# Optimization experiments

Measured on AMD Instinct MI355X. Metric: run time of the kernel, lower is better.

Reference implementation:

```python
import jax, jax.numpy as jnp
import numpy as np

N = 10000        # nodes
E = 320000       # edges (before self-loops)
G = 100          # graphs in batch
HEADS = 2
OUT = 125        # per-head out channels
NEG_SLOPE = 0.2  # PyG GATConv default leaky_relu slope


def setup_inputs() -> dict:
    key = jax.random.key(0)
    k = lambda i: jax.random.fold_in(key, i)
    rn = lambda i, shape, s=0.1: jax.random.normal(k(i), shape, jnp.float32) * s
    inp = {
        "x": jax.random.normal(k(0), (N, 336), jnp.float32),
        "edge_index": jax.random.randint(k(1), (2, E), 0, N, jnp.int32),
        "batch": jnp.sort(jax.random.randint(k(2), (N,), 0, G, jnp.int32)),
    }
    conv_in = [336, 250, 250, 250]
    for i, din in enumerate(conv_in, start=1):
        base = 10 * i
        inp[f"W{i}"] = rn(base, (din, HEADS * OUT))
        inp[f"asrc{i}"] = rn(base + 1, (HEADS, OUT))
        inp[f"adst{i}"] = rn(base + 2, (HEADS, OUT))
        inp[f"b{i}"] = jnp.zeros((HEADS * OUT,), jnp.float32)
    lin_dims = [(250, 200), (200, 100), (100, 100), (100, 29)]
    for i, (din, dout) in enumerate(lin_dims, start=1):
        inp[f"lw{i}"] = rn(100 + i, (din, dout))
        inp[f"lb{i}"] = jnp.zeros((dout,), jnp.float32)
    return inp


def gat_conv(x, src, dst, W, asrc, adst, b):
    # PyG GATConv (v1), concat heads, self-loops already in (src, dst).
    n = x.shape[0]
    h = (x @ W).reshape(n, HEADS, OUT)                    # [N,H,C]
    e_src = jnp.einsum('nhc,hc->nh', h, asrc)             # a_src . h_j
    e_dst = jnp.einsum('nhc,hc->nh', h, adst)             # a_dst . h_i
    e = jax.nn.leaky_relu(e_src[src] + e_dst[dst], NEG_SLOPE)  # [Etot,H]
    m = jax.ops.segment_max(e, dst, num_segments=n)       # segment softmax over incoming edges
    e = jnp.exp(e - m[dst])
    denom = jax.ops.segment_sum(e, dst, num_segments=n)
    alpha = e / (denom[dst] + 1e-16)                      # [Etot,H]
    out = jax.ops.segment_sum(alpha[:, :, None] * h[src], dst, num_segments=n)
    return out.reshape(n, HEADS * OUT) + b


def reference(x, edge_index, batch,
              W1, asrc1, adst1, b1, W2, asrc2, adst2, b2,
              W3, asrc3, adst3, b3, W4, asrc4, adst4, b4,
              lw1, lb1, lw2, lb2, lw3, lb3, lw4, lb4):
    n = x.shape[0]
    loop = jnp.arange(n, dtype=edge_index.dtype)
    src = jnp.concatenate([edge_index[0], loop])          # add_self_loops=True
    dst = jnp.concatenate([edge_index[1], loop])

    h = jax.nn.relu(gat_conv(x, src, dst, W1, asrc1, adst1, b1))
    h = jax.nn.relu(gat_conv(h, src, dst, W2, asrc2, adst2, b2))
    h = jax.nn.relu(gat_conv(h, src, dst, W3, asrc3, adst3, b3))
    h = jax.nn.relu(gat_conv(h, src, dst, W4, asrc4, adst4, b4))

    # global_mean_pool over graph ids
    sums = jax.ops.segment_sum(h, batch, num_segments=G)
    cnts = jax.ops.segment_sum(jnp.ones((n, 1), h.dtype), batch, num_segments=G)
    g = sums / jnp.maximum(cnts, 1.0)                     # [G,250]

    g = jax.nn.relu(g @ lw1 + lb1)
    g = jax.nn.relu(g @ lw2 + lb2)
    g = jax.nn.relu(g @ lw3 + lb3)
    return g @ lw4 + lb4                                  # [G,29]
```

## Files before the change

kernel.cpp:

```cpp
#include <hip/hip_runtime.h>
#include <hip/hip_bf16.h>

#define NNODES 10000
#define NEDGES 320000
#define ETOT   (NEDGES + NNODES)
#define NGRAPH 100
#define CH     250
#define HOUT   125
#define MPAD   10048
#define KP0    352
#define KP1    256
#define HPAD   256
#define DCAP   256

typedef __attribute__((ext_vector_type(8))) short bf16x8;
typedef __attribute__((ext_vector_type(4))) float f32x4;

static __device__ __forceinline__ float bfbits2f(unsigned int u){
  union{ unsigned int i; float f; } v; v.i = u << 16; return v.f;
}
static __device__ __forceinline__ unsigned short f2bfbits(float f){
  __hip_bfloat16 b = __float2bfloat16(f);
  union{ __hip_bfloat16 b; unsigned short s; } v; v.b = b; return v.s;
}

__global__ void k_deg(const int* __restrict__ eidx, int* __restrict__ deg,
                      const int* __restrict__ batch, int* __restrict__ gstart){
  int e = blockIdx.x*blockDim.x + threadIdx.x;
  if (e < ETOT){
    int dst = (e < NEDGES) ? eidx[NEDGES + e] : (e - NEDGES);
    atomicAdd(&deg[dst], 1);
  }
  if (e < NNODES){
    int b1 = batch[e];
    int b0 = (e == 0) ? -1 : batch[e-1];
    for (int b = b0 + 1; b <= b1; ++b) gstart[b] = e;
    if (e == NNODES - 1){
      for (int b = b1 + 1; b <= NGRAPH; ++b) gstart[b] = NNODES;
    }
  }
}

__global__ __launch_bounds__(1024) void k_scan(const int* __restrict__ deg, int* __restrict__ rowptr){
  const int CHUNK = 10;
  int tid = threadIdx.x;
  int base = tid * CHUNK;
  int sum = 0;
  #pragma unroll
  for (int u = 0; u < CHUNK; ++u){
    int i = base + u;
    sum += (i < NNODES) ? deg[i] : 0;
  }
  int lane = tid & 63, wv = tid >> 6;
  int v = sum;
  #pragma unroll
  for (int off = 1; off < 64; off <<= 1){
    int t = __shfl_up(v, off);
    if (lane >= off) v += t;
  }
  __shared__ int wtot[16];
  __shared__ int woff[16];
  if (lane == 63) wtot[wv] = v;
  __syncthreads();
  if (tid == 0){
    int acc = 0;
    #pragma unroll
    for (int w = 0; w < 16; ++w){ woff[w] = acc; acc += wtot[w]; }
  }
  __syncthreads();
  int run = woff[wv] + v - sum;
  #pragma unroll
  for (int u = 0; u < CHUNK; ++u){
    int i = base + u;
    if (i < NNODES){
      run += deg[i];
      rowptr[i+1] = run;
    }
  }
  if (tid == 0) rowptr[0] = 0;
}

__global__ void k_fill(const int* __restrict__ eidx, const int* __restrict__ rowptr,
                       int* __restrict__ cursor, int* __restrict__ csr_src){
  int e = blockIdx.x*blockDim.x + threadIdx.x;
  if (e >= ETOT) return;
  int dst, src;
  if (e < NEDGES){ src = eidx[e]; dst = eidx[NEDGES + e]; }
  else           { src = e - NEDGES; dst = src; }
  int pos = atomicAdd(&cursor[dst], 1);
  csr_src[rowptr[dst] + pos] = src;
}

__global__ void k_xconv(const float* __restrict__ x, __hip_bfloat16* __restrict__ Ab){
  int idx = blockIdx.x*blockDim.x + threadIdx.x;
  if (idx >= NNODES*336) return;
  int r = idx / 336, k = idx % 336;
  Ab[(size_t)r * KP0 + k] = __float2bfloat16(x[idx]);
}

__global__ void k_wconv_all(const float* __restrict__ W0, const float* __restrict__ W1,
                            const float* __restrict__ W2, const float* __restrict__ W3,
                            __hip_bfloat16* __restrict__ Wt0, __hip_bfloat16* __restrict__ Wt1,
                            __hip_bfloat16* __restrict__ Wt2, __hip_bfloat16* __restrict__ Wt3){
  const int T0 = 16 * KP0 * 16;
  const int T1 = 16 * KP1 * 16;
  int idx = blockIdx.x*blockDim.x + threadIdx.x;
  const float* W; __hip_bfloat16* Wt; int K, Kp, li;
  if (idx < T0)              { W = W0; Wt = Wt0; K = 336; Kp = KP0; li = idx; }
  else if (idx < T0 +   T1)  { W = W1; Wt = Wt1; K = CH;  Kp = KP1; li = idx - T0; }
  else if (idx < T0 + 2*T1)  { W = W2; Wt = Wt2; K = CH;  Kp = KP1; li = idx - T0 - T1; }
  else if (idx < T0 + 3*T1)  { W = W3; Wt = Wt3; K = CH;  Kp = KP1; li = idx - T0 - 2*T1; }
  else return;
  int KC = Kp >> 5;
  int nt = li / (Kp * 16);
  int rem = li % (Kp * 16);
  int k = rem / 16;
  int n = rem % 16;
  int col = nt * 16 + n;
  float v = (k < K && col < CH) ? W[(size_t)k * CH + col] : 0.f;
  Wt[(((size_t)nt * KC + (k >> 5)) * 16 + n) * 32 + (k & 31)] = __float2bfloat16(v);
}

__global__ __launch_bounds__(256) void k_gemm_mfma(
    const __hip_bfloat16* __restrict__ A, const __hip_bfloat16* __restrict__ Wt,
    __hip_bfloat16* __restrict__ Cb, const float* __restrict__ asrc,
    const float* __restrict__ adst, float* __restrict__ esrc, float* __restrict__ edst,
    int M, int Kp){
  int wv = threadIdx.x >> 6, lane = threadIdx.x & 63;
  int n16 = lane & 15, q = lane >> 4;
  int KC = Kp >> 5;
  int rowbase = blockIdx.x * 64 + wv * 16;
  int bn = blockIdx.y * 64;
  int nt0 = bn >> 4;
  const __hip_bfloat16* ap = A  + (size_t)(rowbase + n16) * Kp + q * 8;
  const __hip_bfloat16* bp = Wt + ((size_t)nt0 * KC * 16 + n16) * 32 + q * 8;
  f32x4 ac0 = {0.f,0.f,0.f,0.f}, ac1 = ac0, ac2 = ac0, ac3 = ac0;
  for (int kc = 0; kc < KC; ++kc){
    bf16x8 a  = *(const bf16x8*)(ap + (size_t)kc * 32);
    bf16x8 b0 = *(const bf16x8*)(bp + ((size_t)0 * KC + kc) * 512);
    bf16x8 b1 = *(const bf16x8*)(bp + ((size_t)1 * KC + kc) * 512);
    bf16x8 b2 = *(const bf16x8*)(bp + ((size_t)2 * KC + kc) * 512);
    bf16x8 b3 = *(const bf16x8*)(bp + ((size_t)3 * KC + kc) * 512);
    ac0 = __builtin_amdgcn_mfma_f32_16x16x32_bf16(a, b0, ac0, 0, 0, 0);
    ac1 = __builtin_amdgcn_mfma_f32_16x16x32_bf16(a, b1, ac1, 0, 0, 0);
    ac2 = __builtin_amdgcn_mfma_f32_16x16x32_bf16(a, b2, ac2, 0, 0, 0);
    ac3 = __builtin_amdgcn_mfma_f32_16x16x32_bf16(a, b3, ac3, 0, 0, 0);
  }
  float es0[4] = {}, es1[4] = {}, ed0a[4] = {}, ed1a[4] = {};
  #define SCORE_T(AC, T) { \
    int col = bn + (T)*16 + n16; \
    bool ok = col < CH; \
    float av = ok ? asrc[col] : 0.f; \
    float dv = ok ? adst[col] : 0.f; \
    bool hh = col >= HOUT; \
    float av0 = hh ? 0.f : av, av1 = hh ? av : 0.f; \
    float dv0 = hh ? 0.f : dv, dv1 = hh ? dv : 0.f; \
    _Pragma("unroll") \
    for (int r = 0; r < 4; ++r){ \
      es0[r] += AC[r]*av0; es1[r] += AC[r]*av1; \
      ed0a[r] += AC[r]*dv0; ed1a[r] += AC[r]*dv1; } }
  SCORE_T(ac0, 0) SCORE_T(ac1, 1) SCORE_T(ac2, 2) SCORE_T(ac3, 3)
  #undef SCORE_T
  #pragma unroll
  for (int off = 1; off < 16; off <<= 1){
    #pragma unroll
    for (int r = 0; r < 4; ++r){
      es0[r]  += __shfl_xor(es0[r],  off);
      es1[r]  += __shfl_xor(es1[r],  off);
      ed0a[r] += __shfl_xor(ed0a[r], off);
      ed1a[r] += __shfl_xor(ed1a[r], off);
    }
  }
  if (n16 == 0){
    #pragma unroll
    for (int r = 0; r < 4; ++r){
      int row = rowbase + q*4 + r;
      if (row < M){
        atomicAdd(&esrc[row*2+0], es0[r]);
        atomicAdd(&esrc[row*2+1], es1[r]);
        atomicAdd(&edst[row*2+0], ed0a[r]);
        atomicAdd(&edst[row*2+1], ed1a[r]);
      }
    }
  }
  #pragma unroll
  for (int r = 0; r < 4; ++r){
    int row = rowbase + q * 4 + r;
    if (row >= M) continue;
    int col = bn + n16;
    __hip_bfloat16* cb = Cb + (size_t)row * HPAD + col;
    if (col      < CH) cb[0]  = __float2bfloat16(ac0[r]);
    if (col + 16 < CH) cb[16] = __float2bfloat16(ac1[r]);
    if (col + 32 < CH) cb[32] = __float2bfloat16(ac2[r]);
    if (col + 48 < CH) cb[48] = __float2bfloat16(ac3[r]);
  }
}

__global__ __launch_bounds__(256) void k_attn(const __hip_bfloat16* __restrict__ h,
                        const float* __restrict__ esrc, const float* __restrict__ edst,
                        const int* __restrict__ rowptr, const int* __restrict__ csr_src,
                        const float* __restrict__ bias, __hip_bfloat16* __restrict__ outb,
                        float* __restrict__ esZ, float* __restrict__ edZ){
  int node = blockIdx.x;
  int tid = threadIdx.x, wave = tid >> 6, lane = tid & 63;
  int start = rowptr[node], deg = rowptr[node+1] - start;
  __shared__ int   s_src[DCAP];
  __shared__ float s_x0[DCAP], s_x1[DCAP];
  __shared__ float wred0[4], wred1[4];
  __shared__ float sh[4 * 256];
  float ed0 = edst[node*2+0], ed1 = edst[node*2+1];
  float sm0 = 0.f, sm1 = 0.f;
  for (int i = tid; i < deg; i += 256){
    int src = csr_src[start + i];
    float e0 = esrc[src*2+0] + ed0; e0 = e0 > 0.f ? e0 : 0.2f*e0;
    float e1 = esrc[src*2+1] + ed1; e1 = e1 > 0.f ? e1 : 0.2f*e1;
    float x0 = __expf(e0), x1 = __expf(e1);
    if (i < DCAP){ s_src[i] = src; s_x0[i] = x0; s_x1[i] = x1; }
    sm0 += x0; sm1 += x1;
  }
  for (int off = 32; off > 0; off >>= 1){
    sm0 += __shfl_xor(sm0, off);
    sm1 += __shfl_xor(sm1, off);
  }
  if (lane == 0){ wred0[wave] = sm0; wred1[wave] = sm1; }
  __syncthreads();
  float inv0 = 1.f / ((wred0[0]+wred0[1]+wred0[2]+wred0[3]) + 1e-16f);
  float inv1 = 1.f / ((wred1[0]+wred1[1]+wred1[2]+wred1[3]) + 1e-16f);
  int c0 = 4*lane;
  bool h0_0 = (c0    ) < HOUT, h0_1 = (c0 + 1) < HOUT;
  bool h0_2 = (c0 + 2) < HOUT, h0_3 = (c0 + 3) < HOUT;
  float acc0=0.f, acc1=0.f, acc2=0.f, acc3=0.f;
  #define FETCH(I, S, A0, A1) { \
    if ((I) < DCAP){ S = s_src[I]; A0 = s_x0[I]*inv0; A1 = s_x1[I]*inv1; } \
    else { S = csr_src[start + (I)]; \
      float e0 = esrc[S*2+0] + ed0; e0 = e0 > 0.f ? e0 : 0.2f*e0; \
      float e1 = esrc[S*2+1] + ed1; e1 = e1 > 0.f ? e1 : 0.2f*e1; \
      A0 = __expf(e0)*inv0; A1 = __expf(e1)*inv1; } }
  #define GATHER(S, A0, A1) { \
    uint2 d = *(const uint2*)(h + (size_t)(S) * HPAD + c0); \
    acc0 += (h0_0 ? A0 : A1) * bfbits2f(d.x & 0xffffu); \
    acc1 += (h0_1 ? A0 : A1) * bfbits2f(d.x >> 16); \
    acc2 += (h0_2 ? A0 : A1) * bfbits2f(d.y & 0xffffu); \
    acc3 += (h0_3 ? A0 : A1) * bfbits2f(d.y >> 16); }
  int i = wave;
  for (; i + 4 < deg; i += 8){
    int sA, sB; float a0A,a1A,a0B,a1B;
    FETCH(i, sA, a0A, a1A)
    FETCH(i+4, sB, a0B, a1B)
    GATHER(sA, a0A, a1A)
    GATHER(sB, a0B, a1B)
  }
  if (i < deg){
    int sA; float a0A, a1A;
    FETCH(i, sA, a0A, a1A)
    GATHER(sA, a0A, a1A)
  }
  #undef GATHER
  #undef FETCH
  float* shw = sh + wave * 256;
  *(float4*)&shw[c0] = make_float4(acc0, acc1, acc2, acc3);
  __syncthreads();
  if (tid < 62){
    int c = 4*tid;
    float4 b4 = *(const float4*)&bias[c];
    float v0 = sh[c]   + sh[256+c]   + sh[512+c]   + sh[768+c]   + b4.x;
    float v1 = sh[c+1] + sh[256+c+1] + sh[512+c+1] + sh[768+c+1] + b4.y;
    float v2 = sh[c+2] + sh[256+c+2] + sh[512+c+2] + sh[768+c+2] + b4.z;
    float v3 = sh[c+3] + sh[256+c+3] + sh[512+c+3] + sh[768+c+3] + b4.w;
    v0 = v0 > 0.f ? v0 : 0.f; v1 = v1 > 0.f ? v1 : 0.f;
    v2 = v2 > 0.f ? v2 : 0.f; v3 = v3 > 0.f ? v3 : 0.f;
    ushort4 o; o.x = f2bfbits(v0); o.y = f2bfbits(v1); o.z = f2bfbits(v2); o.w = f2bfbits(v3);
    *(ushort4*)(outb + (size_t)node * KP1 + c) = o;
  } else if (tid == 62){
    #pragma unroll
    for (int j = 0; j < 2; ++j){
      int c = 248 + j;
      float v = sh[c] + sh[256+c] + sh[512+c] + sh[768+c] + bias[c];
      v = v > 0.f ? v : 0.f;
      outb[(size_t)node * KP1 + c] = __float2bfloat16(v);
    }
  }
  if (tid < 2){
    esZ[node*2 + tid] = 0.f;
    edZ[node*2 + tid] = 0.f;
  }
}

__global__ __launch_bounds__(256) void k_head(const __hip_bfloat16* __restrict__ xb,
                        const int* __restrict__ gstart,
                        const float* __restrict__ lw1, const float* __restrict__ lb1,
                        const float* __restrict__ lw2, const float* __restrict__ lb2,
                        const float* __restrict__ lw3, const float* __restrict__ lb3,
                        const float* __restrict__ lw4, const float* __restrict__ lb4,
                        float* __restrict__ out){
  int g = blockIdx.x;
  int tid = threadIdx.x;
  int s = gstart[g], e = gstart[g+1];
  __shared__ float gvec[256];
  __shared__ float m1[200];
  __shared__ float m2[112];
  __shared__ float m3[112];
  if (tid < CH){
    float a0=0.f,a1=0.f,a2=0.f,a3=0.f;
    int n = s;
    for (; n + 3 < e; n += 4){
      a0 += __bfloat162float(xb[(size_t)n     * KP1 + tid]);
      a1 += __bfloat162float(xb[(size_t)(n+1) * KP1 + tid]);
      a2 += __bfloat162float(xb[(size_t)(n+2) * KP1 + tid]);
      a3 += __bfloat162float(xb[(size_t)(n+3) * KP1 + tid]);
    }
    for (; n < e; ++n) a0 += __bfloat162float(xb[(size_t)n * KP1 + tid]);
    float scale = 1.f / fmaxf((float)(e - s), 1.f);
    gvec[tid] = (a0 + a1 + a2 + a3) * scale;
  }
  __syncthreads();
  if (tid < 200){
    float a0=0.f,a1=0.f,a2=0.f,a3=0.f;
    int k = 0;
    for (; k + 3 < CH; k += 4){
      a0 += gvec[k]   * lw1[(size_t)k     * 200 + tid];
      a1 += gvec[k+1] * lw1[(size_t)(k+1) * 200 + tid];
      a2 += gvec[k+2] * lw1[(size_t)(k+2) * 200 + tid];
      a3 += gvec[k+3] * lw1[(size_t)(k+3) * 200 + tid];
    }
    for (; k < CH; ++k) a0 += gvec[k] * lw1[(size_t)k * 200 + tid];
    float v = a0 + a1 + a2 + a3 + lb1[tid];
    m1[tid] = v > 0.f ? v : 0.f;
  }
  __syncthreads();
  if (tid < 100){
    float a0=0.f,a1=0.f,a2=0.f,a3=0.f;
    for (int k = 0; k + 3 < 200; k += 4){
      a0 += m1[k]   * lw2[(size_t)k     * 100 + tid];
      a1 += m1[k+1] * lw2[(size_t)(k+1) * 100 + tid];
      a2 += m1[k+2] * lw2[(size_t)(k+2) * 100 + tid];
      a3 += m1[k+3] * lw2[(size_t)(k+3) * 100 + tid];
    }
    float v = a0 + a1 + a2 + a3 + lb2[tid];
    m2[tid] = v > 0.f ? v : 0.f;
  }
  __syncthreads();
  if (tid < 100){
    float a0=0.f,a1=0.f,a2=0.f,a3=0.f;
    for (int k = 0; k + 3 < 100; k += 4){
      a0 += m2[k]   * lw3[(size_t)k     * 100 + tid];
      a1 += m2[k+1] * lw3[(size_t)(k+1) * 100 + tid];
      a2 += m2[k+2] * lw3[(size_t)(k+2) * 100 + tid];
      a3 += m2[k+3] * lw3[(size_t)(k+3) * 100 + tid];
    }
    float v = a0 + a1 + a2 + a3 + lb3[tid];
    m3[tid] = v > 0.f ? v : 0.f;
  }
  __syncthreads();
  if (tid < 29){
    float a0=0.f,a1=0.f,a2=0.f,a3=0.f;
    for (int k = 0; k + 3 < 100; k += 4){
      a0 += m3[k]   * lw4[(size_t)k     * 29 + tid];
      a1 += m3[k+1] * lw4[(size_t)(k+1) * 29 + tid];
      a2 += m3[k+2] * lw4[(size_t)(k+2) * 29 + tid];
      a3 += m3[k+3] * lw4[(size_t)(k+3) * 29 + tid];
    }
    out[(size_t)g * 29 + tid] = a0 + a1 + a2 + a3 + lb4[tid];
  }
}

extern "C" void kernel_launch(void* const* d_in, const int* in_sizes, int n_in,
                              void* d_out, int out_size, void* d_ws, size_t ws_size,
                              hipStream_t stream){
  const float* x   = (const float*)d_in[0];
  const int* eidx  = (const int*)d_in[1];
  const int* batch = (const int*)d_in[2];

  char* ws = (char*)d_ws;
  size_t off = 0;
  auto alloc = [&](size_t bytes)->void*{
    void* p = ws + off;
    off = (off + bytes + 255) & ~(size_t)255;
    return p;
  };
  __hip_bfloat16* hb16 = (__hip_bfloat16*)alloc((size_t)NNODES * HPAD * 2);
  __hip_bfloat16* Abf0 = (__hip_bfloat16*)alloc((size_t)MPAD * KP0 * 2);
  __hip_bfloat16* Abf  = (__hip_bfloat16*)alloc((size_t)MPAD * KP1 * 2);
  __hip_bfloat16* Wt0  = (__hip_bfloat16*)alloc((size_t)16 * KP0 * 16 * 2);
  __hip_bfloat16* Wt1  = (__hip_bfloat16*)alloc((size_t)16 * KP1 * 16 * 2);
  __hip_bfloat16* Wt2  = (__hip_bfloat16*)alloc((size_t)16 * KP1 * 16 * 2);
  __hip_bfloat16* Wt3  = (__hip_bfloat16*)alloc((size_t)16 * KP1 * 16 * 2);
  size_t zbeg = off;
  int*   deg    = (int*)  alloc((size_t)NNODES * 4);
  int*   cursor = (int*)  alloc((size_t)NNODES * 4);
  float* esA  = (float*)alloc((size_t)NNODES * 2 * 4);
  float* edA  = (float*)alloc((size_t)NNODES * 2 * 4);
  float* esB  = (float*)alloc((size_t)NNODES * 2 * 4);
  float* edB  = (float*)alloc((size_t)NNODES * 2 * 4);
  size_t zend = off;
  int*    rowptr  = (int*)   alloc((size_t)(NNODES + 1) * 4);
  int*    csr_src = (int*)   alloc((size_t)ETOT * 4);
  int*    gstart  = (int*)   alloc((size_t)(NGRAPH + 1) * 4);

  hipMemsetAsync(ws + zbeg, 0, zend - zbeg, stream);

  k_deg <<<(ETOT + 255)/256, 256, 0, stream>>>(eidx, deg, batch, gstart);
  k_scan<<<1, 1024, 0, stream>>>(deg, rowptr);
  k_fill<<<(ETOT + 255)/256, 256, 0, stream>>>(eidx, rowptr, cursor, csr_src);

  k_xconv<<<(NNODES*336 + 255)/256, 256, 0, stream>>>(x, Abf0);
  {
    int wtot = 16*KP0*16 + 3*16*KP1*16;
    k_wconv_all<<<(wtot + 255)/256, 256, 0, stream>>>(
        (const float*)d_in[3], (const float*)d_in[7], (const float*)d_in[11], (const float*)d_in[15],
        Wt0, Wt1, Wt2, Wt3);
  }

  const __hip_bfloat16* Wts[4] = {Wt0, Wt1, Wt2, Wt3};
  for (int L = 0; L < 4; ++L){
    const float* as_ = (const float*)d_in[4 + 4*L];
    const float* ad_ = (const float*)d_in[5 + 4*L];
    const float* bb  = (const float*)d_in[6 + 4*L];
    int Kp = (L == 0) ? KP0 : KP1;
    const __hip_bfloat16* Ain = (L == 0) ? Abf0 : Abf;
    float* es  = (L & 1) ? esB : esA;
    float* ed  = (L & 1) ? edB : edA;
    float* esZ = (L & 1) ? esA : esB;
    float* edZ = (L & 1) ? edA : edB;

    dim3 gg(MPAD/64, 4);
    k_gemm_mfma<<<gg, 256, 0, stream>>>(Ain, Wts[L], hb16, as_, ad_, es, ed, NNODES, Kp);
    k_attn<<<NNODES, 256, 0, stream>>>(hb16, es, ed, rowptr, csr_src, bb, Abf, esZ, edZ);
  }

  const float* lw1 = (const float*)d_in[19];
  const float* lb1 = (const float*)d_in[20];
  const float* lw2 = (const float*)d_in[21];
  const float* lb2 = (const float*)d_in[22];
  const float* lw3 = (const float*)d_in[23];
  const float* lb3 = (const float*)d_in[24];
  const float* lw4 = (const float*)d_in[25];
  const float* lb4 = (const float*)d_in[26];

  k_head<<<NGRAPH, 256, 0, stream>>>(Abf, gstart, lw1, lb1, lw2, lb2, lw3, lb3,
                                     lw4, lb4, (float*)d_out);
}
```

Measured before the change: 365.4 us.

## Fuse whole GAT pipeline into one cooperative persistent kernel with grid syncs

Replaces the sequence of about a dozen kernel launches (degree count, scan, CSR fill, conversions, per-layer GEMM and attention, head) with a single cooperative persistent kernel. Stages are separated by grid.sync, and work is distributed by grid-stride loops. The layer-0 GEMM runs concurrently with the single-block scan. This targets launch overhead and inter-kernel gaps. The cost is lower parallelism per stage: the grid is capped at 1024 blocks and attention loops over 10000 nodes, grid barriers add their own cost, and a non-cooperative fallback path is kept.

```diff
diff --git a/kernel.cpp b/kernel.cpp
--- a/kernel.cpp
+++ b/kernel.cpp
@@ -1,13 +1,18 @@
 #include <hip/hip_runtime.h>
+#include <hip/hip_cooperative_groups.h>
 #include <hip/hip_bf16.h>
+
+namespace cg = cooperative_groups;
 
 #define NNODES 10000
 #define NEDGES 320000
 #define ETOT   (NEDGES + NNODES)
 #define NGRAPH 100
+#define NCUS   256
 #define CH     250
 #define HOUT   125
 #define MPAD   10048
+#define NTILE  157
 #define KP0    352
 #define KP1    256
 #define HPAD   256
@@ -24,25 +29,22 @@
   union{ __hip_bfloat16 b; unsigned short s; } v; v.b = b; return v.s;
 }
 
-__global__ void k_deg(const int* __restrict__ eidx, int* __restrict__ deg,
-                      const int* __restrict__ batch, int* __restrict__ gstart){
-  int e = blockIdx.x*blockDim.x + threadIdx.x;
-  if (e < ETOT){
-    int dst = (e < NEDGES) ? eidx[NEDGES + e] : (e - NEDGES);
-    atomicAdd(&deg[dst], 1);
-  }
-  if (e < NNODES){
-    int b1 = batch[e];
-    int b0 = (e == 0) ? -1 : batch[e-1];
-    for (int b = b0 + 1; b <= b1; ++b) gstart[b] = e;
-    if (e == NNODES - 1){
-      for (int b = b1 + 1; b <= NGRAPH; ++b) gstart[b] = NNODES;
-    }
-  }
-}
-
-__global__ __launch_bounds__(1024) void k_scan(const int* __restrict__ deg, int* __restrict__ rowptr){
-  const int CHUNK = 10;
+struct MegaArgs {
+  const float* x; const int* eidx; const int* batch;
+  const float *W0,*W1,*W2,*W3;
+  const float *as0,*ad0,*b0;
+  const float *as1,*ad1,*b1;
+  const float *as2,*ad2,*b2;
+  const float *as3,*ad3,*b3;
+  const float *lw1,*lb1,*lw2,*lb2,*lw3,*lb3,*lw4,*lb4;
+  __hip_bfloat16 *hb16, *Abf0, *Abf, *Wt0, *Wt1, *Wt2, *Wt3;
+  int *deg, *cursor, *rowptr, *csr_src, *gstart;
+  float *esA,*edA,*esB,*edB;
+  float* out;
+};
+
+__device__ void scan256(char* smemc, const int* __restrict__ deg, int* __restrict__ rowptr){
+  const int CHUNK = 40;
   int tid = threadIdx.x;
   int base = tid * CHUNK;
   int sum = 0;
@@ -58,14 +60,14 @@
     int t = __shfl_up(v, off);
     if (lane >= off) v += t;
   }
-  __shared__ int wtot[16];
-  __shared__ int woff[16];
+  int* wtot = (int*)smemc;
+  int* woff = (int*)(smemc + 64);
   if (lane == 63) wtot[wv] = v;
   __syncthreads();
   if (tid == 0){
     int acc = 0;
     #pragma unroll
-    for (int w = 0; w < 16; ++w){ woff[w] = acc; acc += wtot[w]; }
+    for (int w = 0; w < 4; ++w){ woff[w] = acc; acc += wtot[w]; }
   }
   __syncthreads();
   int run = woff[wv] + v - sum;
@@ -80,57 +82,16 @@
   if (tid == 0) rowptr[0] = 0;
 }
 
-__global__ void k_fill(const int* __restrict__ eidx, const int* __restrict__ rowptr,
-                       int* __restrict__ cursor, int* __restrict__ csr_src){
-  int e = blockIdx.x*blockDim.x + threadIdx.x;
-  if (e >= ETOT) return;
-  int dst, src;
-  if (e < NEDGES){ src = eidx[e]; dst = eidx[NEDGES + e]; }
-  else           { src = e - NEDGES; dst = src; }
-  int pos = atomicAdd(&cursor[dst], 1);
-  csr_src[rowptr[dst] + pos] = src;
-}
-
-__global__ void k_xconv(const float* __restrict__ x, __hip_bfloat16* __restrict__ Ab){
-  int idx = blockIdx.x*blockDim.x + threadIdx.x;
-  if (idx >= NNODES*336) return;
-  int r = idx / 336, k = idx % 336;
-  Ab[(size_t)r * KP0 + k] = __float2bfloat16(x[idx]);
-}
-
-__global__ void k_wconv_all(const float* __restrict__ W0, const float* __restrict__ W1,
-                            const float* __restrict__ W2, const float* __restrict__ W3,
-                            __hip_bfloat16* __restrict__ Wt0, __hip_bfloat16* __restrict__ Wt1,
-                            __hip_bfloat16* __restrict__ Wt2, __hip_bfloat16* __restrict__ Wt3){
-  const int T0 = 16 * KP0 * 16;
-  const int T1 = 16 * KP1 * 16;
-  int idx = blockIdx.x*blockDim.x + threadIdx.x;
-  const float* W; __hip_bfloat16* Wt; int K, Kp, li;
-  if (idx < T0)              { W = W0; Wt = Wt0; K = 336; Kp = KP0; li = idx; }
-  else if (idx < T0 +   T1)  { W = W1; Wt = Wt1; K = CH;  Kp = KP1; li = idx - T0; }
-  else if (idx < T0 + 2*T1)  { W = W2; Wt = Wt2; K = CH;  Kp = KP1; li = idx - T0 - T1; }
-  else if (idx < T0 + 3*T1)  { W = W3; Wt = Wt3; K = CH;  Kp = KP1; li = idx - T0 - 2*T1; }
-  else return;
-  int KC = Kp >> 5;
-  int nt = li / (Kp * 16);
-  int rem = li % (Kp * 16);
-  int k = rem / 16;
-  int n = rem % 16;
-  int col = nt * 16 + n;
-  float v = (k < K && col < CH) ? W[(size_t)k * CH + col] : 0.f;
-  Wt[(((size_t)nt * KC + (k >> 5)) * 16 + n) * 32 + (k & 31)] = __float2bfloat16(v);
-}
-
-__global__ __launch_bounds__(256) void k_gemm_mfma(
+__device__ __forceinline__ void gemm_body(int bx, int by,
     const __hip_bfloat16* __restrict__ A, const __hip_bfloat16* __restrict__ Wt,
     __hip_bfloat16* __restrict__ Cb, const float* __restrict__ asrc,
     const float* __restrict__ adst, float* __restrict__ esrc, float* __restrict__ edst,
-    int M, int Kp){
+    int Kp){
   int wv = threadIdx.x >> 6, lane = threadIdx.x & 63;
   int n16 = lane & 15, q = lane >> 4;
   int KC = Kp >> 5;
-  int rowbase = blockIdx.x * 64 + wv * 16;
-  int bn = blockIdx.y * 64;
+  int rowbase = bx * 64 + wv * 16;
+  int bn = by * 64;
   int nt0 = bn >> 4;
   const __hip_bfloat16* ap = A  + (size_t)(rowbase + n16) * Kp + q * 8;
   const __hip_bfloat16* bp = Wt + ((size_t)nt0 * KC * 16 + n16) * 32 + q * 8;
@@ -175,7 +136,7 @@
     #pragma unroll
     for (int r = 0; r < 4; ++r){
       int row = rowbase + q*4 + r;
-      if (row < M){
+      if (row < NNODES){
         atomicAdd(&esrc[row*2+0], es0[r]);
         atomicAdd(&esrc[row*2+1], es1[r]);
         atomicAdd(&edst[row*2+0], ed0a[r]);
@@ -186,7 +147,7 @@
   #pragma unroll
   for (int r = 0; r < 4; ++r){
     int row = rowbase + q * 4 + r;
-    if (row >= M) continue;
+    if (row >= NNODES) continue;
     int col = bn + n16;
     __hip_bfloat16* cb = Cb + (size_t)row * HPAD + col;
     if (col      < CH) cb[0]  = __float2bfloat16(ac0[r]);
@@ -196,18 +157,20 @@
   }
 }
 
-__global__ __launch_bounds__(256) void k_attn(const __hip_bfloat16* __restrict__ h,
-                        const float* __restrict__ esrc, const float* __restrict__ edst,
-                        const int* __restrict__ rowptr, const int* __restrict__ csr_src,
-                        const float* __restrict__ bias, __hip_bfloat16* __restrict__ outb,
-                        float* __restrict__ esZ, float* __restrict__ edZ){
-  int node = blockIdx.x;
+__device__ __forceinline__ void attn_body(int node, char* smemc,
+    const __hip_bfloat16* __restrict__ h, const float* __restrict__ esrc,
+    const float* __restrict__ edst, const int* __restrict__ rowptr,
+    const int* __restrict__ csr_src, const float* __restrict__ bias,
+    __hip_bfloat16* __restrict__ outb, float* __restrict__ esZ, float* __restrict__ edZ){
   int tid = threadIdx.x, wave = tid >> 6, lane = tid & 63;
+  int*   s_src = (int*)  smemc;
+  float* s_x0  = (float*)(smemc + 1024);
+  float* s_x1  = (float*)(smemc + 2048);
+  float* wred0 = (float*)(smemc + 3072);
+  float* wred1 = (float*)(smemc + 3088);
+  float* sh    = (float*)(smemc + 3104);
+  __syncthreads();
   int start = rowptr[node], deg = rowptr[node+1] - start;
-  __shared__ int   s_src[DCAP];
-  __shared__ float s_x0[DCAP], s_x1[DCAP];
-  __shared__ float wred0[4], wred1[4];
-  __shared__ float sh[4 * 256];
   float ed0 = edst[node*2+0], ed1 = edst[node*2+1];
   float sm0 = 0.f, sm1 = 0.f;
   for (int i = tid; i < deg; i += 256){
@@ -286,20 +249,20 @@
   }
 }
 
-__global__ __launch_bounds__(256) void k_head(const __hip_bfloat16* __restrict__ xb,
-                        const int* __restrict__ gstart,
-                        const float* __restrict__ lw1, const float* __restrict__ lb1,
-                        const float* __restrict__ lw2, const float* __restrict__ lb2,
-                        const float* __restrict__ lw3, const float* __restrict__ lb3,
-                        const float* __restrict__ lw4, const float* __restrict__ lb4,
-                        float* __restrict__ out){
-  int g = blockIdx.x;
+__device__ __forceinline__ void head_body(int g, char* smemc,
+    const __hip_bfloat16* __restrict__ xb, const int* __restrict__ gstart,
+    const float* __restrict__ lw1, const float* __restrict__ lb1,
+    const float* __restrict__ lw2, const float* __restrict__ lb2,
+    const float* __restrict__ lw3, const float* __restrict__ lb3,
+    const float* __restrict__ lw4, const float* __restrict__ lb4,
+    float* __restrict__ out){
   int tid = threadIdx.x;
+  float* gvec = (float*)smemc;
+  float* m1   = (float*)(smemc + 1024);
+  float* m2   = (float*)(smemc + 1824);
+  float* m3   = (float*)(smemc + 2272);
+  __syncthreads();
   int s = gstart[g], e = gstart[g+1];
-  __shared__ float gvec[256];
-  __shared__ float m1[200];
-  __shared__ float m2[112];
-  __shared__ float m3[112];
   if (tid < CH){
     float a0=0.f,a1=0.f,a2=0.f,a3=0.f;
     int n = s;
@@ -364,13 +327,131 @@
   }
 }
 
+__device__ __forceinline__ void pre_body(const MegaArgs& a, int gtid, int gstr){
+  for (int e = gtid; e < ETOT; e += gstr){
+    int dst = (e < NEDGES) ? a.eidx[NEDGES + e] : (e - NEDGES);
+    atomicAdd(&a.deg[dst], 1);
+  }
+  for (int n = gtid; n < NNODES; n += gstr){
+    int b1 = a.batch[n];
+    int b0 = (n == 0) ? -1 : a.batch[n-1];
+    for (int b = b0 + 1; b <= b1; ++b) a.gstart[b] = n;
+    if (n == NNODES - 1){
+      for (int b = b1 + 1; b <= NGRAPH; ++b) a.gstart[b] = NNODES;
+    }
+  }
+  for (int i = gtid; i < NNODES*336; i += gstr){
+    int r = i / 336, k = i % 336;
+    a.Abf0[(size_t)r * KP0 + k] = __float2bfloat16(a.x[i]);
+  }
+  const int T0 = 16 * KP0 * 16;
+  const int T1 = 16 * KP1 * 16;
+  int tot = T0 + 3*T1;
+  for (int i = gtid; i < tot; i += gstr){
+    const float* W; __hip_bfloat16* Wt; int K, Kp, li;
+    if (i < T0)             { W = a.W0; Wt = a.Wt0; K = 336; Kp = KP0; li = i; }
+    else if (i < T0 +   T1) { W = a.W1; Wt = a.Wt1; K = CH;  Kp = KP1; li = i - T0; }
+    else if (i < T0 + 2*T1) { W = a.W2; Wt = a.Wt2; K = CH;  Kp = KP1; li = i - T0 - T1; }
+    else                    { W = a.W3; Wt = a.Wt3; K = CH;  Kp = KP1; li = i - T0 - 2*T1; }
+    int KC = Kp >> 5;
+    int nt = li / (Kp * 16);
+    int rem = li % (Kp * 16);
+    int k = rem / 16;
+    int n = rem % 16;
+    int col = nt * 16 + n;
+    float v = (k < K && col < CH) ? W[(size_t)k * CH + col] : 0.f;
+    Wt[(((size_t)nt * KC + (k >> 5)) * 16 + n) * 32 + (k & 31)] = __float2bfloat16(v);
+  }
+}
+__device__ __forceinline__ void fill_body(const MegaArgs& a, int gtid, int gstr){
+  for (int e = gtid; e < ETOT; e += gstr){
+    int dst, src;
+    if (e < NEDGES){ src = a.eidx[e]; dst = a.eidx[NEDGES + e]; }
+    else           { src = e - NEDGES; dst = src; }
+    int pos = atomicAdd(&a.cursor[dst], 1);
+    a.csr_src[a.rowptr[dst] + pos] = src;
+  }
+}
+
+__global__ __launch_bounds__(256, 4) void k_mega(MegaArgs a){
+  cg::grid_group grid = cg::this_grid();
+  __shared__ __align__(16) char smem[7424];
+  int tid = threadIdx.x;
+  int gtid = blockIdx.x * 256 + tid;
+  int gstr = gridDim.x * 256;
+
+  pre_body(a, gtid, gstr);
+  grid.sync();
+
+  if (blockIdx.x == 0){
+    scan256(smem, a.deg, a.rowptr);
+  } else {
+    for (int t = (int)blockIdx.x - 1; t < NTILE*4; t += (int)gridDim.x - 1)
+      gemm_body(t % NTILE, t / NTILE, a.Abf0, a.Wt0, a.hb16, a.as0, a.ad0, a.esA, a.edA, KP0);
+  }
+  grid.sync();
+
+  fill_body(a, gtid, gstr);
+  grid.sync();
+
+  for (int node = blockIdx.x; node < NNODES; node += gridDim.x)
+    attn_body(node, smem, a.hb16, a.esA, a.edA, a.rowptr, a.csr_src, a.b0,
+              a.Abf, a.esB, a.edB);
+  grid.sync();
+
+  const __hip_bfloat16* Wts[3] = {a.Wt1, a.Wt2, a.Wt3};
+  const float* ass[3] = {a.as1, a.as2, a.as3};
+  const float* ads[3] = {a.ad1, a.ad2, a.ad3};
+  const float* bbs[3] = {a.b1, a.b2, a.b3};
+  for (int Lm = 0; Lm < 3; ++Lm){
+    float* es  = (Lm & 1) ? a.esA : a.esB;
+    float* ed  = (Lm & 1) ? a.edA : a.edB;
+    float* esZ = (Lm & 1) ? a.esB : a.esA;
+    float* edZ = (Lm & 1) ? a.edB : a.edA;
+    for (int t = blockIdx.x; t < NTILE*4; t += gridDim.x)
+      gemm_body(t % NTILE, t / NTILE, a.Abf, Wts[Lm], a.hb16, ass[Lm], ads[Lm], es, ed, KP1);
+    grid.sync();
+    for (int node = blockIdx.x; node < NNODES; node += gridDim.x)
+      attn_body(node, smem, a.hb16, es, ed, a.rowptr, a.csr_src, bbs[Lm],
+                a.Abf, esZ, edZ);
+    grid.sync();
+  }
+
+  for (int g = blockIdx.x; g < NGRAPH; g += gridDim.x)
+    head_body(g, smem, a.Abf, a.gstart, a.lw1, a.lb1, a.lw2, a.lb2,
+              a.lw3, a.lb3, a.lw4, a.lb4, a.out);
+}
+
+__global__ void k_pre(MegaArgs a){
+  pre_body(a, blockIdx.x * blockDim.x + threadIdx.x, gridDim.x * blockDim.x);
+}
+__global__ __launch_bounds__(256) void k_scan_s(const int* __restrict__ deg, int* __restrict__ rowptr){
+  __shared__ __align__(16) char smem[128];
+  scan256(smem, deg, rowptr);
+}
+__global__ void k_fill_s(MegaArgs a){
+  fill_body(a, blockIdx.x * blockDim.x + threadIdx.x, gridDim.x * blockDim.x);
+}
+__global__ __launch_bounds__(256) void k_gemm_s(const __hip_bfloat16* A, const __hip_bfloat16* Wt,
+    __hip_bfloat16* Cb, const float* asrc, const float* adst, float* esrc, float* edst, int Kp){
+  gemm_body(blockIdx.x, blockIdx.y, A, Wt, Cb, asrc, adst, esrc, edst, Kp);
+}
+__global__ __launch_bounds__(256) void k_attn_s(const __hip_bfloat16* h, const float* esrc,
+    const float* edst, const int* rowptr, const int* csr_src, const float* bias,
+    __hip_bfloat16* outb, float* esZ, float* edZ){
+  __shared__ __align__(16) char smem[7424];
+  attn_body(blockIdx.x, smem, h, esrc, edst, rowptr, csr_src, bias, outb, esZ, edZ);
+}
+__global__ __launch_bounds__(256) void k_head_s(const __hip_bfloat16* xb, const int* gstart,
+    const float* lw1, const float* lb1, const float* lw2, const float* lb2,
+    const float* lw3, const float* lb3, const float* lw4, const float* lb4, float* out){
+  __shared__ __align__(16) char smem[2720];
+  head_body(blockIdx.x, smem, xb, gstart, lw1, lb1, lw2, lb2, lw3, lb3, lw4, lb4, out);
+}
+
 extern "C" void kernel_launch(void* const* d_in, const int* in_sizes, int n_in,
                               void* d_out, int out_size, void* d_ws, size_t ws_size,
                               hipStream_t stream){
-  const float* x   = (const float*)d_in[0];
-  const int* eidx  = (const int*)d_in[1];
-  const int* batch = (const int*)d_in[2];
-
   char* ws = (char*)d_ws;
   size_t off = 0;
   auto alloc = [&](size_t bytes)->void*{
@@ -393,50 +474,69 @@
   float* esB  = (float*)alloc((size_t)NNODES * 2 * 4);
   float* edB  = (float*)alloc((size_t)NNODES * 2 * 4);
   size_t zend = off;
-  int*    rowptr  = (int*)   alloc((size_t)(NNODES + 1) * 4);
-  int*    csr_src = (int*)   alloc((size_t)ETOT * 4);
-  int*    gstart  = (int*)   alloc((size_t)(NGRAPH + 1) * 4);
+  int*   rowptr  = (int*)alloc((size_t)(NNODES + 1) * 4);
+  int*   csr_src = (int*)alloc((size_t)ETOT * 4);
+  int*   gstart  = (int*)alloc((size_t)(NGRAPH + 1) * 4);
 
   hipMemsetAsync(ws + zbeg, 0, zend - zbeg, stream);
 
-  k_deg <<<(ETOT + 255)/256, 256, 0, stream>>>(eidx, deg, batch, gstart);
-  k_scan<<<1, 1024, 0, stream>>>(deg, rowptr);
-  k_fill<<<(ETOT + 255)/256, 256, 0, stream>>>(eidx, rowptr, cursor, csr_src);
-
-  k_xconv<<<(NNODES*336 + 255)/256, 256, 0, stream>>>(x, Abf0);
-  {
-    int wtot = 16*KP0*16 + 3*16*KP1*16;
-    k_wconv_all<<<(wtot + 255)/256, 256, 0, stream>>>(
-        (const float*)d_in[3], (const float*)d_in[7], (const float*)d_in[11], (const float*)d_in[15],
-        Wt0, Wt1, Wt2, Wt3);
-  }
-
-  const __hip_bfloat16* Wts[4] = {Wt0, Wt1, Wt2, Wt3};
-  for (int L = 0; L < 4; ++L){
-    const float* as_ = (const float*)d_in[4 + 4*L];
-    const float* ad_ = (const float*)d_in[5 + 4*L];
-    const float* bb  = (const float*)d_in[6 + 4*L];
-    int Kp = (L == 0) ? KP0 : KP1;
-    const __hip_bfloat16* Ain = (L == 0) ? Abf0 : Abf;
-    float* es  = (L & 1) ? esB : esA;
-    float* ed  = (L & 1) ? edB : edA;
-    float* esZ = (L & 1) ? esA : esB;
-    float* edZ = (L & 1) ? edA : edB;
-
-    dim3 gg(MPAD/64, 4);
-    k_gemm_mfma<<<gg, 256, 0, stream>>>(Ain, Wts[L], hb16, as_, ad_, es, ed, NNODES, Kp);
-    k_attn<<<NNODES, 256, 0, stream>>>(hb16, es, ed, rowptr, csr_src, bb, Abf, esZ, edZ);
-  }
-
-  const float* lw1 = (const float*)d_in[19];
-  const float* lb1 = (const float*)d_in[20];
-  const float* lw2 = (const float*)d_in[21];
-  const float* lb2 = (const float*)d_in[22];
-  const float* lw3 = (const float*)d_in[23];
-  const float* lb3 = (const float*)d_in[24];
-  const float* lw4 = (const float*)d_in[25];
-  const float* lb4 = (const float*)d_in[26];
-
-  k_head<<<NGRAPH, 256, 0, stream>>>(Abf, gstart, lw1, lb1, lw2, lb2, lw3, lb3,
-                                     lw4, lb4, (float*)d_out);
-}
+  MegaArgs ma;
+  ma.x = (const float*)d_in[0];
+  ma.eidx = (const int*)d_in[1];
+  ma.batch = (const int*)d_in[2];
+  ma.W0 = (const float*)d_in[3];  ma.as0 = (const float*)d_in[4];
+  ma.ad0 = (const float*)d_in[5]; ma.b0  = (const float*)d_in[6];
+  ma.W1 = (const float*)d_in[7];  ma.as1 = (const float*)d_in[8];
+  ma.ad1 = (const float*)d_in[9]; ma.b1  = (const float*)d_in[10];
+  ma.W2 = (const float*)d_in[11]; ma.as2 = (const float*)d_in[12];
+  ma.ad2 = (const float*)d_in[13]; ma.b2 = (const float*)d_in[14];
+  ma.W3 = (const float*)d_in[15]; ma.as3 = (const float*)d_in[16];
+  ma.ad3 = (const float*)d_in[17]; ma.b3 = (const float*)d_in[18];
+  ma.lw1 = (const float*)d_in[19]; ma.lb1 = (const float*)d_in[20];
+  ma.lw2 = (const float*)d_in[21]; ma.lb2 = (const float*)d_in[22];
+  ma.lw3 = (const float*)d_in[23]; ma.lb3 = (const float*)d_in[24];
+  ma.lw4 = (const float*)d_in[25]; ma.lb4 = (const float*)d_in[26];
+  ma.hb16 = hb16; ma.Abf0 = Abf0; ma.Abf = Abf;
+  ma.Wt0 = Wt0; ma.Wt1 = Wt1; ma.Wt2 = Wt2; ma.Wt3 = Wt3;
+  ma.deg = deg; ma.cursor = cursor; ma.rowptr = rowptr;
+  ma.csr_src = csr_src; ma.gstart = gstart;
+  ma.esA = esA; ma.edA = edA; ma.esB = esB; ma.edB = edB;
+  ma.out = (float*)d_out;
+
+  bool coop_done = false;
+  int occ = 0;
+  hipError_t qe = hipOccupancyMaxActiveBlocksPerMultiprocessor(
+      &occ, reinterpret_cast<const void*>(k_mega), 256, 0);
+  if (qe == hipSuccess && occ > 0){
+    long grid = (long)occ * NCUS;
+    if (grid > 1024) grid = 1024;
+    if (grid >= 8){
+      void* kargs[] = { &ma };
+      hipError_t le = hipLaunchCooperativeKernel(
+          reinterpret_cast<void*>(k_mega), dim3((unsigned)grid), dim3(256), kargs, 0, stream);
+      coop_done = (le == hipSuccess);
+    }
+  }
+
+  if (!coop_done){
+    k_pre  <<<(ETOT + 255)/256, 256, 0, stream>>>(ma);
+    k_scan_s<<<1, 256, 0, stream>>>(deg, rowptr);
+    k_fill_s<<<(ETOT + 255)/256, 256, 0, stream>>>(ma);
+    const __hip_bfloat16* Wts[4] = {Wt0, Wt1, Wt2, Wt3};
+    const float* ass[4] = {ma.as0, ma.as1, ma.as2, ma.as3};
+    const float* ads[4] = {ma.ad0, ma.ad1, ma.ad2, ma.ad3};
+    const float* bbs[4] = {ma.b0, ma.b1, ma.b2, ma.b3};
+    for (int L = 0; L < 4; ++L){
+      int Kp = (L == 0) ? KP0 : KP1;
+      const __hip_bfloat16* Ain = (L == 0) ? Abf0 : Abf;
+      float* es  = (L & 1) ? esB : esA;
+      float* ed  = (L & 1) ? edB : edA;
+      float* esZ = (L & 1) ? esA : esB;
+      float* edZ = (L & 1) ? edA : edB;
+      k_gemm_s<<<dim3(NTILE, 4), 256, 0, stream>>>(Ain, Wts[L], hb16, ass[L], ads[L], es, ed, Kp);
+      k_attn_s<<<NNODES, 256, 0, stream>>>(hb16, es, ed, rowptr, csr_src, bbs[L], Abf, esZ, edZ);
+    }
+    k_head_s<<<NGRAPH, 256, 0, stream>>>(Abf, gstart, ma.lw1, ma.lb1, ma.lw2, ma.lb2,
+                                         ma.lw3, ma.lb3, ma.lw4, ma.lb4, (float*)d_out);
+  }
+}
```

Measured after the change: 1.212 ms. 232% more time.
